# Kernel optimization log

Measured on AMD Instinct MI355X. Metric: run time of the kernel, lower is better.

The kernel has to match this reference:

```python
import jax, jax.numpy as jnp
import numpy as np
from jax import lax

E = 32          # num_experts
H = 1024        # hidden_size
I = 512         # expert intermediate_size
IS = 2048       # shared expert intermediate_size
G = 8           # n_group
TOPK_GROUP = 4
TOP_K = 8
SCALE = 2.5     # routed_scaling_factor
T = 1024        # tokens


def setup_inputs() -> dict:
    key = jax.random.key(0)
    ks = jax.random.split(key, 9)
    s = 0.02
    return {
        "hidden_states": jax.random.normal(ks[0], (T, H), jnp.float32),
        "gate_w": jax.random.normal(ks[1], (E, H), jnp.float32) * s,
        "e_bias": jax.random.normal(ks[2], (E,), jnp.float32) * 0.1,
        "w_gate": jax.random.normal(ks[3], (E, H, I), jnp.float32) * s,
        "w_up": jax.random.normal(ks[4], (E, H, I), jnp.float32) * s,
        "w_down": jax.random.normal(ks[5], (E, I, H), jnp.float32) * s,
        "ws_gate": jax.random.normal(ks[6], (H, IS), jnp.float32) * s,
        "ws_up": jax.random.normal(ks[7], (H, IS), jnp.float32) * s,
        "ws_down": jax.random.normal(ks[8], (IS, H), jnp.float32) * s,
    }


def _routing_combine(logits, e_bias):
    # Deepseekv3RoutingImpl.noaux_tc (non-fused reference path)
    scores = jax.nn.sigmoid(logits)                    # [T, E]
    swb = scores + e_bias                              # [T, E]
    swb_g = swb.reshape(-1, G, E // G)                 # [T, G, E/G]
    group_scores = lax.top_k(swb_g, 2)[0].sum(-1)      # sum of top-2 per group
    _, gidx = lax.top_k(group_scores, TOPK_GROUP)      # [T, TOPK_GROUP]
    gmask = jax.nn.one_hot(gidx, G, dtype=swb.dtype).sum(1)   # [T, G]
    smask = jnp.repeat(gmask, E // G, axis=-1)         # [T, E]
    _, tidx = lax.top_k(swb * smask, TOP_K)            # [T, TOP_K]
    emask = jax.nn.one_hot(tidx, E, dtype=scores.dtype).sum(1)
    sc = scores * emask
    combine = sc / (sc.sum(-1, keepdims=True) + 1e-20) * SCALE
    return combine, tidx


def reference(hidden_states, gate_w, e_bias, w_gate, w_up, w_down, ws_gate, ws_up, ws_down):
    x = hidden_states
    # gate: fp32 logits
    logits = x.astype(jnp.float32) @ gate_w.T          # [T, E]
    combine, _ = _routing_combine(logits, e_bias)
    # routed experts (FusedMoE math): per-expert gated MLP, combined by routing weights
    h1 = jnp.einsum('th,ehi->tei', x, w_gate)          # [T, E, I]
    h2 = jnp.einsum('th,ehi->tei', x, w_up)
    act = jax.nn.silu(h1) * h2
    routed = jnp.einsum('tei,te,eih->th', act, combine.astype(x.dtype), w_down)
    # shared expert GatedMLP
    shared = (jax.nn.silu(x @ ws_gate) * (x @ ws_up)) @ ws_down
    return routed + shared
```

## Files before the change

### kernel.cpp

```cpp
#include <hip/hip_runtime.h>
#include <cstdint>
#include <cmath>

#define T_TOK 1024
#define H_DIM 1024
#define E_NUM 32
#define I_DIM 512
#define IS_DIM 2048
#define NCOL_R 16384
#define NCOL_T 18432
#define SCALE_F 2.5f
#define MAXTILES 96

typedef __bf16 bf16x8 __attribute__((ext_vector_type(8)));
typedef float f32x4 __attribute__((ext_vector_type(4)));

typedef __attribute__((address_space(3))) unsigned int lds_u32_t;
typedef __attribute__((address_space(1))) const unsigned int glb_u32_t;

__device__ __forceinline__ unsigned short f2b(float f) {
    union { float f; uint32_t u; } v; v.f = f;
    return (unsigned short)((v.u + 0x7FFFu + ((v.u >> 16) & 1u)) >> 16);
}

__device__ __forceinline__ uint32_t cvt2(float lo, float hi) {
    uint32_t r;
    asm("v_cvt_pk_bf16_f32 %0, %1, %2" : "=v"(r) : "v"(lo), "v"(hi));
    return r;
}

__device__ __forceinline__ void gll16(const unsigned short* g, unsigned short* l) {
    __builtin_amdgcn_global_load_lds((glb_u32_t*)g, (lds_u32_t*)l, 16, 0, 0);
}

__device__ __forceinline__ void routing_wave(const float* __restrict__ x,
                                             const float* __restrict__ gate_w,
                                             const float* __restrict__ e_bias,
                                             float* __restrict__ combine,
                                             int* __restrict__ topk, int t) {
    int l = threadIdx.x & 63;
    int e = l & 31, half = l >> 5;
    const float4* xr = reinterpret_cast<const float4*>(x + (size_t)t * H_DIM + half * 512);
    const float4* wr = reinterpret_cast<const float4*>(gate_w + (size_t)e * H_DIM + half * 512);
    float s = 0.f;
#pragma unroll 8
    for (int j = 0; j < 128; j++) {
        float4 a = xr[j], b = wr[j];
        s += a.x * b.x + a.y * b.y + a.z * b.z + a.w * b.w;
    }
    s += __shfl_xor(s, 32);
    float sg = 1.f / (1.f + expf(-s));
    float swb = sg + e_bias[e];
    float v1 = __shfl_xor(swb, 1), v2 = __shfl_xor(swb, 2), v3 = __shfl_xor(swb, 3);
    float hi01 = fmaxf(swb, v1), lo01 = fminf(swb, v1);
    float hi23 = fmaxf(v2, v3),  lo23 = fminf(v2, v3);
    float gs = fmaxf(hi01, hi23) + fmaxf(fminf(hi01, hi23), fmaxf(lo01, lo23));
    int g = e >> 2;
    int grank = 0;
#pragma unroll
    for (int gg = 0; gg < 8; gg++) {
        float og = __shfl(gs, gg * 4);
        grank += ((og > gs) || (og == gs && gg < g)) ? 1 : 0;
    }
    bool gsel = grank < 4;
    float candv = gsel ? swb : 0.0f;
    int erank = 0;
#pragma unroll
    for (int ee = 0; ee < 32; ee++) {
        float oc = __shfl(candv, ee);
        erank += ((oc > candv) || (oc == candv && ee < e)) ? 1 : 0;
    }
    bool esel = (erank < 8) && (half == 0);
    unsigned long long m = __ballot(esel);
    int idx = __popcll(m & ((1ull << l) - 1ull));
    if (esel) topk[t * 8 + idx] = e;
    float r = esel ? sg : 0.f;
#pragma unroll
    for (int off = 1; off < 64; off <<= 1) r += __shfl_xor(r, off);
    float inv = SCALE_F / (r + 1e-20f);
    if (half == 0) combine[t * E_NUM + e] = esel ? sg * inv : 0.0f;
}

__global__ __launch_bounds__(256)
void prep1_kernel(const float* __restrict__ x, const float* __restrict__ gate_w,
                  const float* __restrict__ e_bias,
                  unsigned short* __restrict__ xb, float* __restrict__ combine,
                  int* __restrict__ topk) {
    int b = blockIdx.x;
    if (b < 256) {
        int t = b * 4 + (threadIdx.x >> 6);
        routing_wave(x, gate_w, e_bias, combine, topk, t);
        return;
    }
    int bb = b - 256;
#pragma unroll
    for (int p = 0; p < 4; p++) {
        int i = bb * 1024 + p * 256 + threadIdx.x;
        float4 v = reinterpret_cast<const float4*>(x)[i];
        uint2 o;
        o.x = cvt2(v.x, v.y);
        o.y = cvt2(v.z, v.w);
        reinterpret_cast<uint2*>(xb)[i] = o;
    }
}

__global__ __launch_bounds__(1024)
void listbuild_kernel(const int* __restrict__ topk, int* __restrict__ meta,
                      int* __restrict__ pair_token, int* __restrict__ slot_of) {
    __shared__ int cnt[E_NUM], start[E_NUM], fill[E_NUM];
    int t = threadIdx.x;
    if (t < E_NUM) cnt[t] = 0;
    __syncthreads();
    int ids[8];
#pragma unroll
    for (int r = 0; r < 8; r++) {
        ids[r] = topk[t * 8 + r];
        atomicAdd(&cnt[ids[r]], 1);
    }
    __syncthreads();
    if (t == 0) {
        int acc = 0;
        for (int e = 0; e < E_NUM; e++) {
            int nt = (cnt[e] + 127) >> 7;
            start[e] = acc * 128;
            fill[e] = 0;
            for (int j = 0; j < nt; j++) meta[1 + acc + j] = e;
            acc += nt;
        }
        meta[0] = acc;
    }
    __syncthreads();
    for (int i = t; i < MAXTILES * 128; i += 1024) pair_token[i] = 0;
    __syncthreads();
#pragma unroll
    for (int r = 0; r < 8; r++) {
        int e = ids[r];
        int s = start[e] + atomicAdd(&fill[e], 1);
        pair_token[s] = t;
        slot_of[t * 8 + r] = s;
    }
}

__global__ __launch_bounds__(256, 4)
void gateup_fused(const unsigned short* __restrict__ xb,
                  const float* __restrict__ w_gate,
                  const float* __restrict__ w_up,
                  const float* __restrict__ ws_gate,
                  const float* __restrict__ ws_up,
                  const float* __restrict__ combine,
                  const int* __restrict__ pair_token,
                  const int* __restrict__ meta,
                  unsigned short* __restrict__ act_s,
                  unsigned short* __restrict__ act_sh) {
    int b = blockIdx.x;
    bool routed = b < 768;
    int tid = threadIdx.x, lane = tid & 63, w = tid >> 6;
    int wr = w >> 1, wc = w & 1;
    __shared__ __align__(16) unsigned short lA[2][128 * 32];
    __shared__ __align__(16) unsigned short lBg[64 * 40];
    __shared__ __align__(16) unsigned short lBu[64 * 40];

    int srow = w * 32 + (lane >> 2);
    int schunk = (lane & 3) * 8;
    int aoff = (w * 32) * 32;
    int nc = (tid & 31) * 2;
    int kg = tid >> 5;

    const unsigned short *gA0, *gA1;
    const float *gBg, *gBu;
    int bstride;
    int e = 0, slot0 = 0, row0 = 0, ci0 = 0;
    if (routed) {
        int tile = b >> 3;
        if (tile >= meta[0]) return;
        e = meta[1 + tile];
        ci0 = (b & 7) * 64;
        slot0 = tile * 128;
        int tok0 = pair_token[slot0 + srow];
        int tok1 = pair_token[slot0 + srow + 16];
        gA0 = xb + (size_t)tok0 * H_DIM + schunk;
        gA1 = xb + (size_t)tok1 * H_DIM + schunk;
        gBg = w_gate + (size_t)e * H_DIM * I_DIM + ci0;
        gBu = w_up   + (size_t)e * H_DIM * I_DIM + ci0;
        bstride = I_DIM;
    } else {
        int bb = b - 768;
        row0 = (bb >> 5) * 128;
        ci0 = (bb & 31) * 64;
        gA0 = xb + (size_t)(row0 + srow) * H_DIM + schunk;
        gA1 = gA0 + 16 * H_DIM;
        gBg = ws_gate + ci0;
        gBu = ws_up + ci0;
        bstride = IS_DIM;
    }

    f32x4 accg[4][2], accu[4][2];
#pragma unroll
    for (int i = 0; i < 4; i++)
#pragma unroll
        for (int j = 0; j < 2; j++)
#pragma unroll
            for (int r = 0; r < 4; r++) { accg[i][j][r] = 0.f; accu[i][j][r] = 0.f; }

    float2 vg[4], vu[4];

#define GU_LOADB(KK)                                                    \
    do {                                                                \
        size_t kb = (size_t)((KK) * 32 + kg * 4);                       \
        _Pragma("unroll")                                               \
        for (int j = 0; j < 4; j++) {                                   \
            vg[j] = *reinterpret_cast<const float2*>(&gBg[(kb + j) * bstride + nc]); \
            vu[j] = *reinterpret_cast<const float2*>(&gBu[(kb + j) * bstride + nc]); \
        }                                                               \
    } while (0)

#define GU_GLLA(KK, BSEL)                                               \
    do {                                                                \
        int _k0 = (KK) * 32;                                            \
        unsigned short* _a = &lA[BSEL][aoff];                           \
        gll16(gA0 + _k0, _a);                                           \
        gll16(gA1 + _k0, _a + 16 * 32);                                 \
    } while (0)

#define GU_WRB()                                                        \
    do {                                                                \
        uint2 u;                                                        \
        u.x = cvt2(vg[0].x, vg[1].x); u.y = cvt2(vg[2].x, vg[3].x);     \
        *reinterpret_cast<uint2*>(&lBg[nc * 40 + kg * 4]) = u;          \
        u.x = cvt2(vg[0].y, vg[1].y); u.y = cvt2(vg[2].y, vg[3].y);     \
        *reinterpret_cast<uint2*>(&lBg[(nc + 1) * 40 + kg * 4]) = u;    \
        u.x = cvt2(vu[0].x, vu[1].x); u.y = cvt2(vu[2].x, vu[3].x);     \
        *reinterpret_cast<uint2*>(&lBu[nc * 40 + kg * 4]) = u;          \
        u.x = cvt2(vu[0].y, vu[1].y); u.y = cvt2(vu[2].y, vu[3].y);     \
        *reinterpret_cast<uint2*>(&lBu[(nc + 1) * 40 + kg * 4]) = u;    \
    } while (0)

    GU_GLLA(0, 0);
    GU_LOADB(0);
    __syncthreads();
    GU_WRB();
    __syncthreads();
    for (int kk = 0; kk < 32; kk++) {
        int cur = kk & 1;
        if (kk < 31) { GU_GLLA(kk + 1, cur ^ 1); GU_LOADB(kk + 1); }
        bf16x8 af[4], bgf[2], buf2[2];
#pragma unroll
        for (int mi = 0; mi < 4; mi++)
            af[mi] = *reinterpret_cast<const bf16x8*>(
                &lA[cur][(wr * 64 + mi * 16 + (lane & 15)) * 32 + (lane >> 4) * 8]);
#pragma unroll
        for (int ni = 0; ni < 2; ni++) {
            int nn = (wc * 32 + ni * 16 + (lane & 15)) * 40 + (lane >> 4) * 8;
            bgf[ni] = *reinterpret_cast<const bf16x8*>(&lBg[nn]);
            buf2[ni] = *reinterpret_cast<const bf16x8*>(&lBu[nn]);
        }
#pragma unroll
        for (int mi = 0; mi < 4; mi++)
#pragma unroll
            for (int ni = 0; ni < 2; ni++) {
                accg[mi][ni] = __builtin_amdgcn_mfma_f32_16x16x32_bf16(af[mi], bgf[ni], accg[mi][ni], 0, 0, 0);
                accu[mi][ni] = __builtin_amdgcn_mfma_f32_16x16x32_bf16(af[mi], buf2[ni], accu[mi][ni], 0, 0, 0);
            }
        __syncthreads();
        if (kk < 31) {
            GU_WRB();
            __syncthreads();
        }
    }
#undef GU_LOADB
#undef GU_GLLA
#undef GU_WRB

    int q = lane >> 4, cl = lane & 15;
    if (routed) {
#pragma unroll
        for (int mi = 0; mi < 4; mi++) {
#pragma unroll
            for (int r = 0; r < 4; r++) {
                int row = wr * 64 + mi * 16 + q * 4 + r;
                int token = pair_token[slot0 + row];
                float s = combine[token * E_NUM + e];
#pragma unroll
                for (int ni = 0; ni < 2; ni++) {
                    float g = accg[mi][ni][r], u = accu[mi][ni][r];
                    float a = g / (1.f + expf(-g)) * u * s;
                    act_s[(size_t)(slot0 + row) * I_DIM + ci0 + wc * 32 + ni * 16 + cl] = f2b(a);
                }
            }
        }
    } else {
#pragma unroll
        for (int mi = 0; mi < 4; mi++) {
#pragma unroll
            for (int ni = 0; ni < 2; ni++) {
                int col = ci0 + wc * 32 + ni * 16 + cl;
#pragma unroll
                for (int r = 0; r < 4; r++) {
                    int row = row0 + wr * 64 + mi * 16 + q * 4 + r;
                    float g = accg[mi][ni][r], u = accu[mi][ni][r];
                    float a = g / (1.f + expf(-g)) * u;
                    act_sh[(size_t)row * IS_DIM + col] = f2b(a);
                }
            }
        }
    }
}

__global__ __launch_bounds__(256, 4)
void down_fused(const unsigned short* __restrict__ act_s,
                const float* __restrict__ w_down,
                const unsigned short* __restrict__ act_sh,
                const float* __restrict__ ws_down,
                const int* __restrict__ meta,
                float* __restrict__ pairpart,
                float* __restrict__ shpart) {
    int b = blockIdx.x;
    bool routed = b < 768;
    int tid = threadIdx.x, lane = tid & 63, w = tid >> 6;
    int wr = w >> 1, wc = w & 1;
    __shared__ __align__(16) unsigned short lA[2][128 * 32];
    __shared__ __align__(16) unsigned short lB[128 * 40];

    int srow = w * 32 + (lane >> 2);
    int schunk = (lane & 3) * 8;
    int aoff = (w * 32) * 32;
    int nc = (tid & 63) * 2;
    int kg = tid >> 6;

    const unsigned short* gA0;
    const float* gB;
    size_t ast;
    int kbase, n0, orow;
    float* outp;
    if (routed) {
        int tile = b >> 3;
        if (tile >= meta[0]) return;
        int e = meta[1 + tile];
        n0 = (b & 7) * 128;
        int slot0 = tile * 128;
        gA0 = act_s + (size_t)(slot0 + srow) * I_DIM + schunk;
        gB = w_down + (size_t)e * I_DIM * H_DIM + n0;
        ast = I_DIM; kbase = 0;
        outp = pairpart; orow = slot0;
    } else {
        int bb = b - 768;
        int mb = bb >> 5, nb = (bb >> 2) & 7, ks = bb & 3;
        int row0 = mb * 128;
        n0 = nb * 128;
        gA0 = act_sh + (size_t)(row0 + srow) * IS_DIM + schunk;
        gB = ws_down + n0;
        ast = IS_DIM; kbase = ks * 512;
        outp = shpart + ((size_t)ks << 20); orow = row0;
    }

    f32x4 acc[4][4];
#pragma unroll
    for (int i = 0; i < 4; i++)
#pragma unroll
        for (int j = 0; j < 4; j++)
#pragma unroll
            for (int r = 0; r < 4; r++) acc[i][j][r] = 0.f;

    float2 vb[8];

#define DN_LOADB(KK)                                                    \
    do {                                                                \
        size_t kb = (size_t)(kbase + (KK) * 32 + kg * 8);               \
        _Pragma("unroll")                                               \
        for (int j = 0; j < 8; j++)                                     \
            vb[j] = *reinterpret_cast<const float2*>(&gB[(kb + j) * H_DIM + nc]); \
    } while (0)

#define DN_GLLA(KK, BSEL)                                               \
    do {                                                                \
        size_t _k0 = (size_t)kbase + (size_t)(KK) * 32;                 \
        unsigned short* _a = &lA[BSEL][aoff];                           \
        gll16(gA0 + _k0, _a);                                           \
        gll16(gA0 + 16 * ast + _k0, _a + 16 * 32);                      \
    } while (0)

#define DN_WRB()                                                        \
    do {                                                                \
        uint4 u;                                                        \
        u.x = cvt2(vb[0].x, vb[1].x); u.y = cvt2(vb[2].x, vb[3].x);     \
        u.z = cvt2(vb[4].x, vb[5].x); u.w = cvt2(vb[6].x, vb[7].x);     \
        *reinterpret_cast<uint4*>(&lB[nc * 40 + kg * 8]) = u;           \
        u.x = cvt2(vb[0].y, vb[1].y); u.y = cvt2(vb[2].y, vb[3].y);     \
        u.z = cvt2(vb[4].y, vb[5].y); u.w = cvt2(vb[6].y, vb[7].y);     \
        *reinterpret_cast<uint4*>(&lB[(nc + 1) * 40 + kg * 8]) = u;     \
    } while (0)

    DN_GLLA(0, 0);
    DN_LOADB(0);
    __syncthreads();
    DN_WRB();
    __syncthreads();
    for (int kk = 0; kk < 16; kk++) {
        int cur = kk & 1;
        if (kk < 15) { DN_GLLA(kk + 1, cur ^ 1); DN_LOADB(kk + 1); }
        bf16x8 af[4], bf[4];
#pragma unroll
        for (int mi = 0; mi < 4; mi++)
            af[mi] = *reinterpret_cast<const bf16x8*>(
                &lA[cur][(wr * 64 + mi * 16 + (lane & 15)) * 32 + (lane >> 4) * 8]);
#pragma unroll
        for (int ni = 0; ni < 4; ni++)
            bf[ni] = *reinterpret_cast<const bf16x8*>(
                &lB[(wc * 64 + ni * 16 + (lane & 15)) * 40 + (lane >> 4) * 8]);
#pragma unroll
        for (int mi = 0; mi < 4; mi++)
#pragma unroll
            for (int ni = 0; ni < 4; ni++)
                acc[mi][ni] = __builtin_amdgcn_mfma_f32_16x16x32_bf16(af[mi], bf[ni], acc[mi][ni], 0, 0, 0);
        __syncthreads();
        if (kk < 15) {
            DN_WRB();
            __syncthreads();
        }
    }
#undef DN_LOADB
#undef DN_GLLA
#undef DN_WRB

    int q = lane >> 4, cl = lane & 15;
#pragma unroll
    for (int mi = 0; mi < 4; mi++) {
#pragma unroll
        for (int ni = 0; ni < 4; ni++) {
            int col = n0 + wc * 64 + ni * 16 + cl;
#pragma unroll
            for (int r = 0; r < 4; r++) {
                int row = orow + wr * 64 + mi * 16 + q * 4 + r;
                outp[(size_t)row * H_DIM + col] = acc[mi][ni][r];
            }
        }
    }
}

__global__ void final_combine(const float* __restrict__ pairpart,
                              const float* __restrict__ shpart,
                              const int* __restrict__ slot_of,
                              float* __restrict__ out) {
    int t = blockIdx.x;
    int h = threadIdx.x * 4;
    float4 o = reinterpret_cast<const float4*>(shpart + (size_t)t * H_DIM + h)[0];
#pragma unroll
    for (int ks = 1; ks < 4; ks++) {
        float4 v = reinterpret_cast<const float4*>(shpart + ((size_t)ks << 20) + (size_t)t * H_DIM + h)[0];
        o.x += v.x; o.y += v.y; o.z += v.z; o.w += v.w;
    }
#pragma unroll
    for (int r = 0; r < 8; r++) {
        int s = slot_of[t * 8 + r];
        float4 v = reinterpret_cast<const float4*>(pairpart + (size_t)s * H_DIM + h)[0];
        o.x += v.x; o.y += v.y; o.z += v.z; o.w += v.w;
    }
    reinterpret_cast<float4*>(out + (size_t)t * H_DIM + h)[0] = o;
}


__global__ void cvt_x_kernel(const float* __restrict__ x, unsigned short* __restrict__ xb) {
    int i = blockIdx.x * 256 + threadIdx.x;
    float4 v = reinterpret_cast<const float4*>(x)[i];
    uint2 o;
    o.x = (uint32_t)f2b(v.x) | ((uint32_t)f2b(v.y) << 16);
    o.y = (uint32_t)f2b(v.z) | ((uint32_t)f2b(v.w) << 16);
    reinterpret_cast<uint2*>(xb)[i] = o;
}

__global__ void routing_kernel(const float* __restrict__ x,
                               const float* __restrict__ gate_w,
                               const float* __restrict__ e_bias,
                               float* __restrict__ combine,
                               int* __restrict__ topk) {
    int t = blockIdx.x;
    routing_wave(x, gate_w, e_bias, combine, topk, t);
}

__global__ __launch_bounds__(256, 2)
void gateup_kernel(const unsigned short* __restrict__ xb,
                   const float* __restrict__ w_gate,
                   const float* __restrict__ w_up,
                   const float* __restrict__ ws_gate,
                   const float* __restrict__ ws_up,
                   const float* __restrict__ combine,
                   unsigned short* __restrict__ act) {
    int mb = blockIdx.x, cb = blockIdx.y;
    int row0 = mb * 128, c0 = cb * 128;
    const float *bg, *bu;
    int bstride, eidx;
    if (c0 < NCOL_R) {
        int e = c0 >> 9, ci = c0 & 511;
        bg = w_gate + (size_t)e * H_DIM * I_DIM + ci;
        bu = w_up   + (size_t)e * H_DIM * I_DIM + ci;
        bstride = I_DIM; eidx = e;
    } else {
        int ci = c0 - NCOL_R;
        bg = ws_gate + ci; bu = ws_up + ci;
        bstride = IS_DIM; eidx = -1;
    }
    __shared__ __align__(16) unsigned short lA[128*32];
    __shared__ __align__(16) unsigned short lBg[128*32];
    __shared__ __align__(16) unsigned short lBu[128*32];
    int tid = threadIdx.x, lane = tid & 63, w = tid >> 6;
    int wr = w >> 1, wc = w & 1;
    f32x4 accg[4][4], accu[4][4];
#pragma unroll
    for (int i = 0; i < 4; i++)
#pragma unroll
        for (int j = 0; j < 4; j++)
#pragma unroll
            for (int r = 0; r < 4; r++) { accg[i][j][r] = 0.f; accu[i][j][r] = 0.f; }
    int ar = tid >> 2, ak = (tid & 3) * 8;
    int bn = tid & 127, bkg = (tid >> 7) * 16;
    for (int kk = 0; kk < H_DIM / 32; kk++) {
        int k0 = kk * 32;
        __syncthreads();
        *reinterpret_cast<uint4*>(&lA[ar*32 + ak]) =
            *reinterpret_cast<const uint4*>(xb + (size_t)(row0 + ar) * H_DIM + k0 + ak);
        *reinterpret_cast<uint4*>(&lA[(ar+64)*32 + ak]) =
            *reinterpret_cast<const uint4*>(xb + (size_t)(row0 + ar + 64) * H_DIM + k0 + ak);
#pragma unroll
        for (int p = 0; p < 4; p++) {
            int kb = bkg + p * 4;
            const float* pg = bg + (size_t)(k0 + kb) * bstride + bn;
            uint2 dg;
            dg.x = (uint32_t)f2b(pg[0])         | ((uint32_t)f2b(pg[bstride])   << 16);
            dg.y = (uint32_t)f2b(pg[2*bstride]) | ((uint32_t)f2b(pg[3*bstride]) << 16);
            *reinterpret_cast<uint2*>(&lBg[bn*32 + kb]) = dg;
            const float* pu = bu + (size_t)(k0 + kb) * bstride + bn;
            uint2 du;
            du.x = (uint32_t)f2b(pu[0])         | ((uint32_t)f2b(pu[bstride])   << 16);
            du.y = (uint32_t)f2b(pu[2*bstride]) | ((uint32_t)f2b(pu[3*bstride]) << 16);
            *reinterpret_cast<uint2*>(&lBu[bn*32 + kb]) = du;
        }
        __syncthreads();
        bf16x8 af[4], bgf[4], buf2[4];
#pragma unroll
        for (int mi = 0; mi < 4; mi++)
            af[mi] = *reinterpret_cast<const bf16x8*>(&lA[(wr*64 + mi*16 + (lane & 15))*32 + (lane >> 4)*8]);
#pragma unroll
        for (int ni = 0; ni < 4; ni++) {
            int nn = (wc*64 + ni*16 + (lane & 15))*32 + (lane >> 4)*8;
            bgf[ni]  = *reinterpret_cast<const bf16x8*>(&lBg[nn]);
            buf2[ni] = *reinterpret_cast<const bf16x8*>(&lBu[nn]);
        }
#pragma unroll
        for (int mi = 0; mi < 4; mi++)
#pragma unroll
            for (int ni = 0; ni < 4; ni++) {
                accg[mi][ni] = __builtin_amdgcn_mfma_f32_16x16x32_bf16(af[mi], bgf[ni],  accg[mi][ni], 0, 0, 0);
                accu[mi][ni] = __builtin_amdgcn_mfma_f32_16x16x32_bf16(af[mi], buf2[ni], accu[mi][ni], 0, 0, 0);
            }
    }
    int q = lane >> 4, cl = lane & 15;
#pragma unroll
    for (int mi = 0; mi < 4; mi++) {
#pragma unroll
        for (int ni = 0; ni < 4; ni++) {
            int colg = c0 + wc*64 + ni*16 + cl;
#pragma unroll
            for (int r = 0; r < 4; r++) {
                int row = row0 + wr*64 + mi*16 + q*4 + r;
                float g = accg[mi][ni][r], u = accu[mi][ni][r];
                float a = g / (1.f + expf(-g)) * u;
                float s = (eidx >= 0) ? combine[row * E_NUM + eidx] : 1.0f;
                act[(size_t)row * NCOL_T + colg] = f2b(a * s);
            }
        }
    }
}

__global__ __launch_bounds__(256, 2)
void down_kernel(const unsigned short* __restrict__ act,
                 const float* __restrict__ w_down,
                 const float* __restrict__ ws_down,
                 float* __restrict__ partials) {
    int mb = blockIdx.x, nb = blockIdx.y, ks = blockIdx.z;
    int row0 = mb * 128, n0 = nb * 128;
    __shared__ __align__(16) unsigned short lA[128*32];
    __shared__ __align__(16) unsigned short lB[128*32];
    int tid = threadIdx.x, lane = tid & 63, w = tid >> 6;
    int wr = w >> 1, wc = w & 1;
    f32x4 acc[4][4];
#pragma unroll
    for (int i = 0; i < 4; i++)
#pragma unroll
        for (int j = 0; j < 4; j++)
#pragma unroll
            for (int r = 0; r < 4; r++) acc[i][j][r] = 0.f;
    int ar = tid >> 2, ak = (tid & 3) * 8;
    int bn = tid & 127, bkg = (tid >> 7) * 16;
    for (int kk = 0; kk < 144; kk++) {
        int k0 = ks * 4608 + kk * 32;
        const float* bb = (k0 < NCOL_R) ? (w_down + (size_t)k0 * H_DIM)
                                        : (ws_down + (size_t)(k0 - NCOL_R) * H_DIM);
        __syncthreads();
        *reinterpret_cast<uint4*>(&lA[ar*32 + ak]) =
            *reinterpret_cast<const uint4*>(act + (size_t)(row0 + ar) * NCOL_T + k0 + ak);
        *reinterpret_cast<uint4*>(&lA[(ar+64)*32 + ak]) =
            *reinterpret_cast<const uint4*>(act + (size_t)(row0 + ar + 64) * NCOL_T + k0 + ak);
#pragma unroll
        for (int p = 0; p < 4; p++) {
            int kb = bkg + p * 4;
            const float* pb = bb + (size_t)kb * H_DIM + n0 + bn;
            uint2 d;
            d.x = (uint32_t)f2b(pb[0])       | ((uint32_t)f2b(pb[H_DIM])   << 16);
            d.y = (uint32_t)f2b(pb[2*H_DIM]) | ((uint32_t)f2b(pb[3*H_DIM]) << 16);
            *reinterpret_cast<uint2*>(&lB[bn*32 + kb]) = d;
        }
        __syncthreads();
        bf16x8 af[4], bf[4];
#pragma unroll
        for (int mi = 0; mi < 4; mi++)
            af[mi] = *reinterpret_cast<const bf16x8*>(&lA[(wr*64 + mi*16 + (lane & 15))*32 + (lane >> 4)*8]);
#pragma unroll
        for (int ni = 0; ni < 4; ni++)
            bf[ni] = *reinterpret_cast<const bf16x8*>(&lB[(wc*64 + ni*16 + (lane & 15))*32 + (lane >> 4)*8]);
#pragma unroll
        for (int mi = 0; mi < 4; mi++)
#pragma unroll
            for (int ni = 0; ni < 4; ni++)
                acc[mi][ni] = __builtin_amdgcn_mfma_f32_16x16x32_bf16(af[mi], bf[ni], acc[mi][ni], 0, 0, 0);
    }
    float* pout = partials + ((size_t)ks << 20);
    int q = lane >> 4, cl = lane & 15;
#pragma unroll
    for (int mi = 0; mi < 4; mi++) {
#pragma unroll
        for (int ni = 0; ni < 4; ni++) {
            int col = n0 + wc*64 + ni*16 + cl;
#pragma unroll
            for (int r = 0; r < 4; r++) {
                int row = row0 + wr*64 + mi*16 + q*4 + r;
                pout[(size_t)row * H_DIM + col] = acc[mi][ni][r];
            }
        }
    }
}

__global__ void reduce_kernel(const float* __restrict__ p, float* __restrict__ out) {
    int i = blockIdx.x * 256 + threadIdx.x;
    float4 a = reinterpret_cast<const float4*>(p)[i];
    float4 b = reinterpret_cast<const float4*>(p + (size_t)1048576)[i];
    float4 c = reinterpret_cast<const float4*>(p + (size_t)2097152)[i];
    float4 d = reinterpret_cast<const float4*>(p + (size_t)3145728)[i];
    float4 o;
    o.x = a.x + b.x + c.x + d.x;
    o.y = a.y + b.y + c.y + d.y;
    o.z = a.z + b.z + c.z + d.z;
    o.w = a.w + b.w + c.w + d.w;
    reinterpret_cast<float4*>(out)[i] = o;
}

extern "C" void kernel_launch(void* const* d_in, const int* in_sizes, int n_in,
                              void* d_out, int out_size, void* d_ws, size_t ws_size,
                              hipStream_t stream) {
    const float* x       = (const float*)d_in[0];
    const float* gate_w  = (const float*)d_in[1];
    const float* e_bias  = (const float*)d_in[2];
    const float* w_gate  = (const float*)d_in[3];
    const float* w_up    = (const float*)d_in[4];
    const float* w_down  = (const float*)d_in[5];
    const float* ws_gate = (const float*)d_in[6];
    const float* ws_up   = (const float*)d_in[7];
    const float* ws_down = (const float*)d_in[8];
    float* out = (float*)d_out;

    char* ws = (char*)d_ws;
    bool fast = ws_size >= 170000384ull;

    if (fast) {
        float* combine      = (float*)(ws);
        int*   topk         = (int*)(ws + 131072);
        int*   meta         = (int*)(ws + 163840);
        int*   pair_token   = (int*)(ws + 164352);
        int*   slot_of      = (int*)(ws + 213504);
        unsigned short* xb  = (unsigned short*)(ws + 262144);
        unsigned short* act_s  = (unsigned short*)(ws + 2359296);
        unsigned short* act_sh = (unsigned short*)(ws + 14942208);
        float* pairpart     = (float*)(ws + 19136512);
        float* shpart       = (float*)(ws + 69468160);

        prep1_kernel<<<512, 256, 0, stream>>>(x, gate_w, e_bias, xb, combine, topk);
        listbuild_kernel<<<1, 1024, 0, stream>>>(topk, meta, pair_token, slot_of);
        gateup_fused<<<1024, 256, 0, stream>>>(xb, w_gate, w_up, ws_gate, ws_up,
                                               combine, pair_token, meta, act_s, act_sh);
        down_fused<<<1024, 256, 0, stream>>>(act_s, w_down, act_sh, ws_down, meta,
                                             pairpart, shpart);
        final_combine<<<1024, 256, 0, stream>>>(pairpart, shpart, slot_of, out);
    } else {
        float* combine     = (float*)(ws);
        int*   topk        = (int*)(ws + 131072);
        unsigned short* xb = (unsigned short*)(ws + 262144);
        unsigned short* act= (unsigned short*)(ws + 2359296);
        float* partials    = (float*)(ws + 40108032);

        cvt_x_kernel<<<1024, 256, 0, stream>>>(x, xb);
        routing_kernel<<<1024, 64, 0, stream>>>(x, gate_w, e_bias, combine, topk);
        gateup_kernel<<<dim3(8, 144), 256, 0, stream>>>(xb, w_gate, w_up, ws_gate, ws_up, combine, act);
        down_kernel<<<dim3(8, 8, 4), 256, 0, stream>>>(act, w_down, ws_down, partials);
        reduce_kernel<<<1024, 256, 0, stream>>>(partials, out);
    }
}
```

Measured before the change: 341.3 us.

## Drop LDS staging in MoE GEMMs; load MFMA fragments directly from global

Rewrites the gate/up and down GEMM kernels so each lane loads its A fragment (bf16) and B fragment (fp32, converted to bf16 in registers) straight from global memory, with no LDS tiles, no double buffering and no __syncthreads. Launch bounds drop to 3 blocks per CU to leave room for the extra registers. This removes LDS write/read traffic and barrier stalls. In exchange, A and B data shared across waves is no longer reused through LDS, the B loads become scalar 4-byte strided reads instead of wider vector loads, and software prefetch of the next k-step is lost, so the kernel leans on L1/L2 and on occupancy to hide latency.

```diff
diff --git a/kernel.cpp b/kernel.cpp
--- a/kernel.cpp
+++ b/kernel.cpp
@@ -29,8 +29,13 @@
     return r;
 }
 
-__device__ __forceinline__ void gll16(const unsigned short* g, unsigned short* l) {
-    __builtin_amdgcn_global_load_lds((glb_u32_t*)g, (lds_u32_t*)l, 16, 0, 0);
+__device__ __forceinline__ bf16x8 mkfrag(const float f[8]) {
+    union { uint32_t u[4]; bf16x8 v; } r;
+    r.u[0] = cvt2(f[0], f[1]);
+    r.u[1] = cvt2(f[2], f[3]);
+    r.u[2] = cvt2(f[4], f[5]);
+    r.u[3] = cvt2(f[6], f[7]);
+    return r.v;
 }
 
 __device__ __forceinline__ void routing_wave(const float* __restrict__ x,
@@ -141,7 +146,7 @@
     }
 }
 
-__global__ __launch_bounds__(256, 4)
+__global__ __launch_bounds__(256, 3)
 void gateup_fused(const unsigned short* __restrict__ xb,
                   const float* __restrict__ w_gate,
                   const float* __restrict__ w_up,
@@ -156,43 +161,47 @@
     bool routed = b < 768;
     int tid = threadIdx.x, lane = tid & 63, w = tid >> 6;
     int wr = w >> 1, wc = w & 1;
-    __shared__ __align__(16) unsigned short lA[2][128 * 32];
-    __shared__ __align__(16) unsigned short lBg[64 * 40];
-    __shared__ __align__(16) unsigned short lBu[64 * 40];
-
-    int srow = w * 32 + (lane >> 2);
-    int schunk = (lane & 3) * 8;
-    int aoff = (w * 32) * 32;
-    int nc = (tid & 31) * 2;
-    int kg = tid >> 5;
-
-    const unsigned short *gA0, *gA1;
-    const float *gBg, *gBu;
+    int q = lane >> 4, cl = lane & 15;
+
+    const char *bgc, *buc;
     int bstride;
     int e = 0, slot0 = 0, row0 = 0, ci0 = 0;
+    uint32_t arow[4];
     if (routed) {
         int tile = b >> 3;
         if (tile >= meta[0]) return;
         e = meta[1 + tile];
         ci0 = (b & 7) * 64;
         slot0 = tile * 128;
-        int tok0 = pair_token[slot0 + srow];
-        int tok1 = pair_token[slot0 + srow + 16];
-        gA0 = xb + (size_t)tok0 * H_DIM + schunk;
-        gA1 = xb + (size_t)tok1 * H_DIM + schunk;
-        gBg = w_gate + (size_t)e * H_DIM * I_DIM + ci0;
-        gBu = w_up   + (size_t)e * H_DIM * I_DIM + ci0;
+#pragma unroll
+        for (int mi = 0; mi < 4; mi++) {
+            int row = wr * 64 + mi * 16 + cl;
+            int token = pair_token[slot0 + row];
+            arow[mi] = (uint32_t)token * (H_DIM * 2) + q * 16;
+        }
+        bgc = reinterpret_cast<const char*>(w_gate + (size_t)e * H_DIM * I_DIM);
+        buc = reinterpret_cast<const char*>(w_up   + (size_t)e * H_DIM * I_DIM);
         bstride = I_DIM;
     } else {
         int bb = b - 768;
         row0 = (bb >> 5) * 128;
         ci0 = (bb & 31) * 64;
-        gA0 = xb + (size_t)(row0 + srow) * H_DIM + schunk;
-        gA1 = gA0 + 16 * H_DIM;
-        gBg = ws_gate + ci0;
-        gBu = ws_up + ci0;
+#pragma unroll
+        for (int mi = 0; mi < 4; mi++) {
+            int row = row0 + wr * 64 + mi * 16 + cl;
+            arow[mi] = (uint32_t)row * (H_DIM * 2) + q * 16;
+        }
+        bgc = reinterpret_cast<const char*>(ws_gate);
+        buc = reinterpret_cast<const char*>(ws_up);
         bstride = IS_DIM;
     }
+    const char* xbc = reinterpret_cast<const char*>(xb);
+    uint32_t colb = (uint32_t)(ci0 + wc * 32 + cl) * 4;
+    uint32_t boff[8];
+#pragma unroll
+    for (int j = 0; j < 8; j++)
+        boff[j] = (uint32_t)(q * 8 + j) * bstride * 4 + colb;
+    uint32_t binc = (uint32_t)(32 * bstride * 4);
 
     f32x4 accg[4][2], accu[4][2];
 #pragma unroll
@@ -202,76 +211,34 @@
 #pragma unroll
             for (int r = 0; r < 4; r++) { accg[i][j][r] = 0.f; accu[i][j][r] = 0.f; }
 
-    float2 vg[4], vu[4];
-
-#define GU_LOADB(KK)                                                    \
-    do {                                                                \
-        size_t kb = (size_t)((KK) * 32 + kg * 4);                       \
-        _Pragma("unroll")                                               \
-        for (int j = 0; j < 4; j++) {                                   \
-            vg[j] = *reinterpret_cast<const float2*>(&gBg[(kb + j) * bstride + nc]); \
-            vu[j] = *reinterpret_cast<const float2*>(&gBu[(kb + j) * bstride + nc]); \
-        }                                                               \
-    } while (0)
-
-#define GU_GLLA(KK, BSEL)                                               \
-    do {                                                                \
-        int _k0 = (KK) * 32;                                            \
-        unsigned short* _a = &lA[BSEL][aoff];                           \
-        gll16(gA0 + _k0, _a);                                           \
-        gll16(gA1 + _k0, _a + 16 * 32);                                 \
-    } while (0)
-
-#define GU_WRB()                                                        \
-    do {                                                                \
-        uint2 u;                                                        \
-        u.x = cvt2(vg[0].x, vg[1].x); u.y = cvt2(vg[2].x, vg[3].x);     \
-        *reinterpret_cast<uint2*>(&lBg[nc * 40 + kg * 4]) = u;          \
-        u.x = cvt2(vg[0].y, vg[1].y); u.y = cvt2(vg[2].y, vg[3].y);     \
-        *reinterpret_cast<uint2*>(&lBg[(nc + 1) * 40 + kg * 4]) = u;    \
-        u.x = cvt2(vu[0].x, vu[1].x); u.y = cvt2(vu[2].x, vu[3].x);     \
-        *reinterpret_cast<uint2*>(&lBu[nc * 40 + kg * 4]) = u;          \
-        u.x = cvt2(vu[0].y, vu[1].y); u.y = cvt2(vu[2].y, vu[3].y);     \
-        *reinterpret_cast<uint2*>(&lBu[(nc + 1) * 40 + kg * 4]) = u;    \
-    } while (0)
-
-    GU_GLLA(0, 0);
-    GU_LOADB(0);
-    __syncthreads();
-    GU_WRB();
-    __syncthreads();
+    uint32_t abump = 0;
     for (int kk = 0; kk < 32; kk++) {
-        int cur = kk & 1;
-        if (kk < 31) { GU_GLLA(kk + 1, cur ^ 1); GU_LOADB(kk + 1); }
-        bf16x8 af[4], bgf[2], buf2[2];
+        float g0[8], g1[8], u0[8], u1[8];
+#pragma unroll
+        for (int j = 0; j < 8; j++) {
+            g0[j] = *reinterpret_cast<const float*>(bgc + boff[j]);
+            g1[j] = *reinterpret_cast<const float*>(bgc + boff[j] + 64);
+            u0[j] = *reinterpret_cast<const float*>(buc + boff[j]);
+            u1[j] = *reinterpret_cast<const float*>(buc + boff[j] + 64);
+        }
+        bf16x8 af[4];
 #pragma unroll
         for (int mi = 0; mi < 4; mi++)
-            af[mi] = *reinterpret_cast<const bf16x8*>(
-                &lA[cur][(wr * 64 + mi * 16 + (lane & 15)) * 32 + (lane >> 4) * 8]);
-#pragma unroll
-        for (int ni = 0; ni < 2; ni++) {
-            int nn = (wc * 32 + ni * 16 + (lane & 15)) * 40 + (lane >> 4) * 8;
-            bgf[ni] = *reinterpret_cast<const bf16x8*>(&lBg[nn]);
-            buf2[ni] = *reinterpret_cast<const bf16x8*>(&lBu[nn]);
-        }
-#pragma unroll
-        for (int mi = 0; mi < 4; mi++)
-#pragma unroll
-            for (int ni = 0; ni < 2; ni++) {
-                accg[mi][ni] = __builtin_amdgcn_mfma_f32_16x16x32_bf16(af[mi], bgf[ni], accg[mi][ni], 0, 0, 0);
-                accu[mi][ni] = __builtin_amdgcn_mfma_f32_16x16x32_bf16(af[mi], buf2[ni], accu[mi][ni], 0, 0, 0);
-            }
-        __syncthreads();
-        if (kk < 31) {
-            GU_WRB();
-            __syncthreads();
-        }
-    }
-#undef GU_LOADB
-#undef GU_GLLA
-#undef GU_WRB
-
-    int q = lane >> 4, cl = lane & 15;
+            af[mi] = *reinterpret_cast<const bf16x8*>(xbc + arow[mi] + abump);
+        abump += 64;
+#pragma unroll
+        for (int j = 0; j < 8; j++) boff[j] += binc;
+        bf16x8 fg0 = mkfrag(g0), fg1 = mkfrag(g1);
+        bf16x8 fu0 = mkfrag(u0), fu1 = mkfrag(u1);
+#pragma unroll
+        for (int mi = 0; mi < 4; mi++) {
+            accg[mi][0] = __builtin_amdgcn_mfma_f32_16x16x32_bf16(af[mi], fg0, accg[mi][0], 0, 0, 0);
+            accg[mi][1] = __builtin_amdgcn_mfma_f32_16x16x32_bf16(af[mi], fg1, accg[mi][1], 0, 0, 0);
+            accu[mi][0] = __builtin_amdgcn_mfma_f32_16x16x32_bf16(af[mi], fu0, accu[mi][0], 0, 0, 0);
+            accu[mi][1] = __builtin_amdgcn_mfma_f32_16x16x32_bf16(af[mi], fu1, accu[mi][1], 0, 0, 0);
+        }
+    }
+
     if (routed) {
 #pragma unroll
         for (int mi = 0; mi < 4; mi++) {
@@ -306,7 +273,7 @@
     }
 }
 
-__global__ __launch_bounds__(256, 4)
+__global__ __launch_bounds__(256, 3)
 void down_fused(const unsigned short* __restrict__ act_s,
                 const float* __restrict__ w_down,
                 const unsigned short* __restrict__ act_sh,
@@ -318,19 +285,11 @@
     bool routed = b < 768;
     int tid = threadIdx.x, lane = tid & 63, w = tid >> 6;
     int wr = w >> 1, wc = w & 1;
-    __shared__ __align__(16) unsigned short lA[2][128 * 32];
-    __shared__ __align__(16) unsigned short lB[128 * 40];
-
-    int srow = w * 32 + (lane >> 2);
-    int schunk = (lane & 3) * 8;
-    int aoff = (w * 32) * 32;
-    int nc = (tid & 63) * 2;
-    int kg = tid >> 6;
-
-    const unsigned short* gA0;
-    const float* gB;
-    size_t ast;
-    int kbase, n0, orow;
+    int q = lane >> 4, cl = lane & 15;
+
+    const char *gac, *gbc;
+    uint32_t arow[4];
+    int n0, orow, kb0 = 0;
     float* outp;
     if (routed) {
         int tile = b >> 3;
@@ -338,20 +297,35 @@
         int e = meta[1 + tile];
         n0 = (b & 7) * 128;
         int slot0 = tile * 128;
-        gA0 = act_s + (size_t)(slot0 + srow) * I_DIM + schunk;
-        gB = w_down + (size_t)e * I_DIM * H_DIM + n0;
-        ast = I_DIM; kbase = 0;
+#pragma unroll
+        for (int mi = 0; mi < 4; mi++) {
+            int row = slot0 + wr * 64 + mi * 16 + cl;
+            arow[mi] = (uint32_t)row * (I_DIM * 2) + q * 16;
+        }
+        gac = reinterpret_cast<const char*>(act_s);
+        gbc = reinterpret_cast<const char*>(w_down + (size_t)e * I_DIM * H_DIM);
         outp = pairpart; orow = slot0;
     } else {
         int bb = b - 768;
         int mb = bb >> 5, nb = (bb >> 2) & 7, ks = bb & 3;
         int row0 = mb * 128;
         n0 = nb * 128;
-        gA0 = act_sh + (size_t)(row0 + srow) * IS_DIM + schunk;
-        gB = ws_down + n0;
-        ast = IS_DIM; kbase = ks * 512;
+        kb0 = ks * 512;
+#pragma unroll
+        for (int mi = 0; mi < 4; mi++) {
+            int row = row0 + wr * 64 + mi * 16 + cl;
+            arow[mi] = (uint32_t)row * (IS_DIM * 2) + (kb0 + q * 8) * 2;
+        }
+        gac = reinterpret_cast<const char*>(act_sh);
+        gbc = reinterpret_cast<const char*>(ws_down);
         outp = shpart + ((size_t)ks << 20); orow = row0;
     }
+    uint32_t colb = (uint32_t)(n0 + wc * 64 + cl) * 4;
+    uint32_t boff[8];
+#pragma unroll
+    for (int j = 0; j < 8; j++)
+        boff[j] = (uint32_t)(kb0 + q * 8 + j) * (H_DIM * 4) + colb;
+    const uint32_t binc = 32u * H_DIM * 4;
 
     f32x4 acc[4][4];
 #pragma unroll
@@ -361,68 +335,33 @@
 #pragma unroll
             for (int r = 0; r < 4; r++) acc[i][j][r] = 0.f;
 
-    float2 vb[8];
-
-#define DN_LOADB(KK)                                                    \
-    do {                                                                \
-        size_t kb = (size_t)(kbase + (KK) * 32 + kg * 8);               \
-        _Pragma("unroll")                                               \
-        for (int j = 0; j < 8; j++)                                     \
-            vb[j] = *reinterpret_cast<const float2*>(&gB[(kb + j) * H_DIM + nc]); \
-    } while (0)
-
-#define DN_GLLA(KK, BSEL)                                               \
-    do {                                                                \
-        size_t _k0 = (size_t)kbase + (size_t)(KK) * 32;                 \
-        unsigned short* _a = &lA[BSEL][aoff];                           \
-        gll16(gA0 + _k0, _a);                                           \
-        gll16(gA0 + 16 * ast + _k0, _a + 16 * 32);                      \
-    } while (0)
-
-#define DN_WRB()                                                        \
-    do {                                                                \
-        uint4 u;                                                        \
-        u.x = cvt2(vb[0].x, vb[1].x); u.y = cvt2(vb[2].x, vb[3].x);     \
-        u.z = cvt2(vb[4].x, vb[5].x); u.w = cvt2(vb[6].x, vb[7].x);     \
-        *reinterpret_cast<uint4*>(&lB[nc * 40 + kg * 8]) = u;           \
-        u.x = cvt2(vb[0].y, vb[1].y); u.y = cvt2(vb[2].y, vb[3].y);     \
-        u.z = cvt2(vb[4].y, vb[5].y); u.w = cvt2(vb[6].y, vb[7].y);     \
-        *reinterpret_cast<uint4*>(&lB[(nc + 1) * 40 + kg * 8]) = u;     \
-    } while (0)
-
-    DN_GLLA(0, 0);
-    DN_LOADB(0);
-    __syncthreads();
-    DN_WRB();
-    __syncthreads();
+    uint32_t abump = 0;
     for (int kk = 0; kk < 16; kk++) {
-        int cur = kk & 1;
-        if (kk < 15) { DN_GLLA(kk + 1, cur ^ 1); DN_LOADB(kk + 1); }
-        bf16x8 af[4], bf[4];
+        float b0[8], b1[8], b2[8], b3[8];
+#pragma unroll
+        for (int j = 0; j < 8; j++) {
+            b0[j] = *reinterpret_cast<const float*>(gbc + boff[j]);
+            b1[j] = *reinterpret_cast<const float*>(gbc + boff[j] + 64);
+            b2[j] = *reinterpret_cast<const float*>(gbc + boff[j] + 128);
+            b3[j] = *reinterpret_cast<const float*>(gbc + boff[j] + 192);
+        }
+        bf16x8 af[4];
 #pragma unroll
         for (int mi = 0; mi < 4; mi++)
-            af[mi] = *reinterpret_cast<const bf16x8*>(
-                &lA[cur][(wr * 64 + mi * 16 + (lane & 15)) * 32 + (lane >> 4) * 8]);
-#pragma unroll
-        for (int ni = 0; ni < 4; ni++)
-            bf[ni] = *reinterpret_cast<const bf16x8*>(
-                &lB[(wc * 64 + ni * 16 + (lane & 15)) * 40 + (lane >> 4) * 8]);
-#pragma unroll
-        for (int mi = 0; mi < 4; mi++)
-#pragma unroll
-            for (int ni = 0; ni < 4; ni++)
-                acc[mi][ni] = __builtin_amdgcn_mfma_f32_16x16x32_bf16(af[mi], bf[ni], acc[mi][ni], 0, 0, 0);
-        __syncthreads();
-        if (kk < 15) {
-            DN_WRB();
-            __syncthreads();
-        }
-    }
-#undef DN_LOADB
-#undef DN_GLLA
-#undef DN_WRB
-
-    int q = lane >> 4, cl = lane & 15;
+            af[mi] = *reinterpret_cast<const bf16x8*>(gac + arow[mi] + abump);
+        abump += 64;
+#pragma unroll
+        for (int j = 0; j < 8; j++) boff[j] += binc;
+        bf16x8 f0 = mkfrag(b0), f1 = mkfrag(b1), f2 = mkfrag(b2), f3 = mkfrag(b3);
+#pragma unroll
+        for (int mi = 0; mi < 4; mi++) {
+            acc[mi][0] = __builtin_amdgcn_mfma_f32_16x16x32_bf16(af[mi], f0, acc[mi][0], 0, 0, 0);
+            acc[mi][1] = __builtin_amdgcn_mfma_f32_16x16x32_bf16(af[mi], f1, acc[mi][1], 0, 0, 0);
+            acc[mi][2] = __builtin_amdgcn_mfma_f32_16x16x32_bf16(af[mi], f2, acc[mi][2], 0, 0, 0);
+            acc[mi][3] = __builtin_amdgcn_mfma_f32_16x16x32_bf16(af[mi], f3, acc[mi][3], 0, 0, 0);
+        }
+    }
+
 #pragma unroll
     for (int mi = 0; mi < 4; mi++) {
 #pragma unroll
```

Result: slower. 418.0 us (+22.5%).
